# Performance work log

Hardware: AMD Instinct MI355X
Metric: run time of the kernel (lower is better)

Reference implementation:

```python
import jax, jax.numpy as jnp
import numpy as np

B, S, IN_DIM, D_MODEL, H = 8, 1024, 512, 1024, 16
DEPTH = D_MODEL // H
LN_EPS = 1e-5


def setup_inputs() -> dict:
    key = jax.random.key(0)
    ks = jax.random.split(key, 10)
    def xavier(k, shape):
        fan_in, fan_out = shape[0], shape[1]
        lim = float(np.sqrt(6.0 / (fan_in + fan_out)))
        return jax.random.uniform(k, shape, jnp.float32, -lim, lim)
    return {
        "x": jax.random.normal(ks[0], (B, S, IN_DIM), jnp.float32),
        "mask": jax.random.randint(ks[1], (H, S, S), 0, 2, jnp.int32),
        "wq_w": xavier(ks[2], (IN_DIM, D_MODEL)),
        "wq_b": jnp.zeros((D_MODEL,), jnp.float32),
        "wk_w": xavier(ks[3], (IN_DIM, D_MODEL)),
        "wk_b": jnp.zeros((D_MODEL,), jnp.float32),
        "wv_w": xavier(ks[4], (IN_DIM, D_MODEL)),
        "wv_b": jnp.zeros((D_MODEL,), jnp.float32),
        "dense_w": xavier(ks[5], (D_MODEL, D_MODEL)),
        "dense_b": jnp.zeros((D_MODEL,), jnp.float32),
        "res_w": xavier(ks[6], (IN_DIM, D_MODEL)),  # residual_linear (no bias)
        "ln_g": 1.0 + 0.02 * jax.random.normal(ks[7], (D_MODEL,), jnp.float32),
        "ln_b": 0.02 * jax.random.normal(ks[8], (D_MODEL,), jnp.float32),
    }


def reference(x, mask, wq_w, wq_b, wk_w, wk_b, wv_w, wv_b,
              dense_w, dense_b, res_w, ln_g, ln_b):
    bs = x.shape[0]
    residual = x @ res_w  # [B,S,D_MODEL]
    # project and split heads -> [B,H,S,depth]
    def split(t):
        return t.reshape(bs, -1, H, DEPTH).transpose(0, 2, 1, 3)
    q = split(x @ wq_w + wq_b)
    k = split(x @ wk_w + wk_b)
    v = split(x @ wv_w + wv_b)
    scale = 1.0 / jnp.sqrt(jnp.asarray(DEPTH, x.dtype))
    attn = jnp.einsum("bhqd,bhkd->bhqk", q, k) * scale
    attn = jnp.where(mask[None] == 0, jnp.asarray(-1e9, attn.dtype), attn)
    attn = jax.nn.softmax(attn, axis=-1)  # dropout is identity in eval
    out = jnp.einsum("bhqk,bhkd->bhqd", attn, v)
    out = out.transpose(0, 2, 1, 3).reshape(bs, -1, D_MODEL)
    out = out @ dense_w + dense_b
    # residual + LayerNorm
    y = residual + out
    mu = jnp.mean(y, axis=-1, keepdims=True)
    var = jnp.mean(jnp.square(y - mu), axis=-1, keepdims=True)
    y = (y - mu) * jax.lax.rsqrt(var + LN_EPS)
    return y * ln_g + ln_b
```

## Files before the change

### kernel.cpp

```cpp
#include <hip/hip_runtime.h>
#include <stdint.h>

#define B_ 8
#define S_ 1024
#define IN_DIM 512
#define DM 1024
#define H_ 16
#define DEP 64

typedef __bf16 bf16;
typedef __attribute__((ext_vector_type(8))) __bf16 bf16x8;
typedef __attribute__((ext_vector_type(4))) __bf16 bf16x4;
typedef __attribute__((ext_vector_type(4))) short short4v;
typedef __attribute__((ext_vector_type(4))) float f32x4;

#if defined(__has_builtin)
#if __has_builtin(__builtin_amdgcn_mfma_f32_16x16x16_bf16)
#define HAVE_NEW16 1
#endif
#endif
static __device__ __forceinline__ f32x4 mfma16(bf16x4 a, bf16x4 b, f32x4 c) {
#ifdef HAVE_NEW16
    return __builtin_amdgcn_mfma_f32_16x16x16_bf16(a, b, c, 0, 0, 0);
#else
    union { bf16x4 h; short4v s; } ua, ub;
    ua.h = a; ub.h = b;
    return __builtin_amdgcn_mfma_f32_16x16x16bf16_1k(ua.s, ub.s, c, 0, 0, 0);
#endif
}

static __device__ __forceinline__ void gld_lds16(const void* g, void* l) {
    __builtin_amdgcn_global_load_lds(
        (const __attribute__((address_space(1))) uint32_t*)g,
        (__attribute__((address_space(3))) uint32_t*)l, 16, 0, 0);
}

__global__ void detect_kernel(const uint16_t* __restrict__ xraw, int* __restrict__ flag) {
    const int t = threadIdx.x;
    int sane = 0;
    #pragma unroll
    for (int j = 0; j < 8; j++) {
        const uint16_t u = xraw[t * 8 + j];
        const int e = (u >> 7) & 0xff;
        sane += ((u & 0x7fff) == 0 || (e >= 100 && e <= 140)) ? 1 : 0;
    }
    #pragma unroll
    for (int m = 1; m < 64; m <<= 1) sane += __shfl_xor(sane, m);
    if (t == 0) *flag = (sane >= 450) ? 1 : 0;
}

static __device__ __forceinline__ float ldin(const void* p, size_t i, int isb) {
    return isb ? (float)((const bf16*)p)[i] : ((const float*)p)[i];
}

__global__ __launch_bounds__(256) void transpose_kernel(
    const void* __restrict__ wq, const void* __restrict__ wk, const void* __restrict__ wv,
    const void* __restrict__ res, const void* __restrict__ dense,
    bf16* __restrict__ wqT, bf16* __restrict__ wkT, bf16* __restrict__ wvT,
    bf16* __restrict__ resT, bf16* __restrict__ denseT, const int* __restrict__ flag)
{
    const int isb = *flag;
    __shared__ bf16 tile[32][33];
    const int z = blockIdx.z;
    const void* src; bf16* dst; int kb, kd;
    if (z == 0)      { src = wq;    dst = wqT;    kb = 0;   kd = 512;  }
    else if (z == 1) { src = wk;    dst = wkT;    kb = 0;   kd = 512;  }
    else if (z == 2) { src = wv;    dst = wvT;    kb = 0;   kd = 512;  }
    else if (z == 3) { src = res;   dst = resT;   kb = 0;   kd = 512;  }
    else if (z == 4) { src = dense; dst = denseT; kb = 0;   kd = 1024; }
    else             { src = dense; dst = denseT; kb = 512; kd = 1024; }
    const int n0 = blockIdx.x * 32, k0 = blockIdx.y * 32;
    const int tx = threadIdx.x, ty = threadIdx.y;
    #pragma unroll
    for (int r = 0; r < 4; r++)
        tile[ty + r*8][tx] = (bf16)ldin(src, (size_t)(kb + k0 + ty + r*8) * DM + n0 + tx, isb);
    __syncthreads();
    #pragma unroll
    for (int r = 0; r < 4; r++)
        dst[(size_t)(n0 + ty + r*8) * kd + kb + k0 + tx] = tile[tx][ty + r*8];
}

__global__ __launch_bounds__(256) void xconv_kernel(
    const void* __restrict__ x, bf16* __restrict__ xc, const int* __restrict__ flag)
{
    const int isb = *flag;
    const size_t i = ((size_t)blockIdx.x * 256 + threadIdx.x) * 4;
    #pragma unroll
    for (int j = 0; j < 4; j++) xc[i + j] = (bf16)ldin(x, i + j, isb);
}

__global__ __launch_bounds__(256) void smallconv_kernel(
    const void* b0, const void* b1, const void* b2, const void* b3,
    const void* b4, const void* b5, bf16* __restrict__ out, const int* __restrict__ flag)
{
    const int isb = *flag;
    const void* srcs[6] = {b0, b1, b2, b3, b4, b5};
    const void* s = srcs[blockIdx.x];
    for (int i = threadIdx.x; i < 1024; i += 256)
        out[blockIdx.x * 1024 + i] = (bf16)ldin(s, i, isb);
}

__global__ __launch_bounds__(256) void maskpack_kernel(
    const int* __restrict__ mask, unsigned long long* __restrict__ mb)
{
    const int w = threadIdx.x >> 6, lane = threadIdx.x & 63;
    const int gw = blockIdx.x * 4 + w;
    for (int c = gw; c < 262144; c += 4096) {
        const int v = mask[(size_t)c * 64 + lane];
        const unsigned long long bits = __ballot(v != 0);
        if (lane == 0) mb[c] = bits;
    }
}

template<int KDIM>
static __device__ __forceinline__ void gemm_core(
    const bf16* __restrict__ A, const bf16* __restrict__ BT,
    int m0, int n0, bf16* Asm, bf16* Bsm, f32x4 acc[4][4])
{
    const int tid = threadIdx.x, l = tid & 63, w = tid >> 6;
    const int wm = w >> 1, wn = w & 1, quad = l >> 4, l15 = l & 15;
    #pragma unroll
    for (int i = 0; i < 4; i++)
        #pragma unroll
        for (int j = 0; j < 4; j++) acc[i][j] = f32x4{0.f, 0.f, 0.f, 0.f};

    for (int k0 = 0; k0 < KDIM; k0 += 32) {
        __syncthreads();
        #pragma unroll
        for (int qq = 0; qq < 2; qq++) {
            const int c = qq*256 + tid;
            const int row = c >> 2, ch = c & 3;
            gld_lds16(A  + (size_t)(m0 + row)*KDIM + k0 + ch*8, Asm + (qq*256 + w*64)*8);
            gld_lds16(BT + (size_t)(n0 + row)*KDIM + k0 + ch*8, Bsm + (qq*256 + w*64)*8);
        }
        __syncthreads();
        bf16x8 af[4], bfv[4];
        #pragma unroll
        for (int i = 0; i < 4; i++)
            af[i] = *(const bf16x8*)(Asm + (wm*64 + i*16 + l15)*32 + quad*8);
        #pragma unroll
        for (int j = 0; j < 4; j++)
            bfv[j] = *(const bf16x8*)(Bsm + (wn*64 + j*16 + l15)*32 + quad*8);
        #pragma unroll
        for (int i = 0; i < 4; i++)
            #pragma unroll
            for (int j = 0; j < 4; j++)
                acc[i][j] = __builtin_amdgcn_mfma_f32_16x16x32_bf16(af[i], bfv[j], acc[i][j], 0, 0, 0);
    }
}

#define EPI_P 132
__global__ __launch_bounds__(256) void proj_kernel(
    const bf16* __restrict__ x,
    const bf16* __restrict__ wqT, const bf16* __restrict__ wkT,
    const bf16* __restrict__ wvT, const bf16* __restrict__ resT,
    const bf16* __restrict__ small,
    bf16* __restrict__ Q, bf16* __restrict__ K, bf16* __restrict__ VtG, bf16* __restrict__ R)
{
    __shared__ alignas(16) char smem[17408];
    bf16* Asm = (bf16*)smem;
    bf16* Bsm = (bf16*)(smem + 8192);
    bf16* epi = (bf16*)smem;

    const int m0 = blockIdx.x * 128;
    const int ng = blockIdx.y * 128;
    const int sel = ng >> 10, n0 = ng & 1023;
    const bf16* BT; const bf16* bias = nullptr;
    if (sel == 0)      { BT = wqT; bias = small;        }
    else if (sel == 1) { BT = wkT; bias = small + 1024; }
    else if (sel == 2) { BT = wvT; bias = small + 2048; }
    else               { BT = resT; }

    f32x4 acc[4][4];
    gemm_core<IN_DIM>(x, BT, m0, n0, Asm, Bsm, acc);

    const int tid = threadIdx.x, l = tid & 63, w = tid >> 6;
    const int wm = w >> 1, wn = w & 1, quad = l >> 4, l15 = l & 15;

    if (sel == 2) {
        const int bb = m0 >> 10, srow0 = m0 & 1023;
        #pragma unroll
        for (int hf = 0; hf < 2; hf++) {
            __syncthreads();
            if (wn == hf) {
                #pragma unroll
                for (int j = 0; j < 4; j++) {
                    const int cl = j*16 + l15;
                    const float bv = (float)bias[n0 + hf*64 + cl];
                    #pragma unroll
                    for (int i = 0; i < 4; i++) {
                        const int rho = wm*64 + i*16 + quad*4;
                        #pragma unroll
                        for (int r = 0; r < 4; r++)
                            epi[cl*EPI_P + rho + r] = (bf16)(acc[i][j][r] + bv);
                    }
                }
            }
            __syncthreads();
            const int hh = (n0 >> 6) + hf;
            const int sc = tid & 15;
            #pragma unroll
            for (int pass = 0; pass < 4; pass++) {
                const int dl = (tid >> 4) + pass*16;
                bf16x8 v;
                #pragma unroll
                for (int k = 0; k < 8; k++) v[k] = epi[dl*EPI_P + sc*8 + k];
                *(bf16x8*)(VtG + ((size_t)(bb*16 + hh)*64 + dl)*S_ + srow0 + sc*8) = v;
            }
        }
        return;
    }

    #pragma unroll
    for (int j = 0; j < 4; j++) {
        const int col = n0 + wn*64 + j*16 + l15;
        const float bv = (sel < 3) ? (float)bias[col] : 0.f;
        #pragma unroll
        for (int i = 0; i < 4; i++) {
            const int rb = m0 + wm*64 + i*16 + quad*4;
            #pragma unroll
            for (int r = 0; r < 4; r++) {
                const float v = acc[i][j][r] + bv;
                if (sel == 0)      Q[(size_t)(rb + r)*DM + col] = (bf16)(v * 0.125f);
                else if (sel == 1) K[(size_t)(rb + r)*DM + col] = (bf16)v;
                else               R[(size_t)(rb + r)*DM + col] = (bf16)v;
            }
        }
    }
}

#define KP 68
__global__ __launch_bounds__(256) void attn_kernel(
    const bf16* __restrict__ Q, const bf16* __restrict__ K, const bf16* __restrict__ VtG,
    const unsigned long long* __restrict__ mb, bf16* __restrict__ AO)
{
    __shared__ alignas(16) bf16 Ksm[64*KP];
    __shared__ alignas(16) bf16 Vsm[64*KP];

    const int tid = threadIdx.x, l = tid & 63, w = tid >> 6;
    const int quad = l >> 4, l15 = l & 15;
    const int b = blockIdx.y >> 4, h = blockIdx.y & 15;
    const int wrow = blockIdx.x*128 + w*32;
    const size_t rowbase = (size_t)b * S_;

    bf16x8 qa[2][2];
    #pragma unroll
    for (int g = 0; g < 2; g++) {
        const bf16* qp = Q + (rowbase + wrow + g*16 + l15)*DM + h*DEP + quad*8;
        qa[g][0] = *(const bf16x8*)qp;
        qa[g][1] = *(const bf16x8*)(qp + 32);
    }
    const bf16* kgbase = K + rowbase*DM + h*DEP;
    const bf16* vgbase = VtG + (size_t)(b*16 + h)*64*S_;
    const unsigned long long* mbase[2];
    #pragma unroll
    for (int g = 0; g < 2; g++)
        mbase[g] = mb + ((size_t)h*S_ + wrow + g*16 + l15) * 16;

    f32x4 oT[2][4];
    float lsum[2] = {0.f, 0.f};
    #pragma unroll
    for (int g = 0; g < 2; g++)
        #pragma unroll
        for (int dt = 0; dt < 4; dt++) oT[g][dt] = f32x4{0.f,0.f,0.f,0.f};

    const int srow = tid >> 3, sch = tid & 7;

    bf16x8 k0v = *(const bf16x8*)(kgbase + (size_t)srow*DM + sch*8);
    bf16x8 k1v = *(const bf16x8*)(kgbase + (size_t)(32 + srow)*DM + sch*8);
    bf16x8 v0v = *(const bf16x8*)(vgbase + (size_t)srow*S_ + sch*8);
    bf16x8 v1v = *(const bf16x8*)(vgbase + (size_t)(32 + srow)*S_ + sch*8);
    uint32_t mlo[2], mhi[2];
    #pragma unroll
    for (int g = 0; g < 2; g++) {
        const unsigned long long mword = mbase[g][0];
        mlo[g] = (uint32_t)mword; mhi[g] = (uint32_t)(mword >> 32);
    }

    for (int it = 0; it < 16; it++) {
        __syncthreads();
        *(bf16x8*)(Ksm + srow*KP + sch*8)        = k0v;
        *(bf16x8*)(Ksm + (32 + srow)*KP + sch*8) = k1v;
        *(bf16x8*)(Vsm + srow*KP + sch*8)        = v0v;
        *(bf16x8*)(Vsm + (32 + srow)*KP + sch*8) = v1v;
        __syncthreads();

        const uint32_t cmlo[2] = {mlo[0], mlo[1]}, cmhi[2] = {mhi[0], mhi[1]};
        if (it + 1 < 16) {
            const int nkt = (it + 1) * 64;
            k0v = *(const bf16x8*)(kgbase + (size_t)(nkt + srow)*DM + sch*8);
            k1v = *(const bf16x8*)(kgbase + (size_t)(nkt + 32 + srow)*DM + sch*8);
            v0v = *(const bf16x8*)(vgbase + (size_t)srow*S_ + nkt + sch*8);
            v1v = *(const bf16x8*)(vgbase + (size_t)(32 + srow)*S_ + nkt + sch*8);
            #pragma unroll
            for (int g = 0; g < 2; g++) {
                const unsigned long long mword = mbase[g][it + 1];
                mlo[g] = (uint32_t)mword; mhi[g] = (uint32_t)(mword >> 32);
            }
        }

        #pragma unroll
        for (int sub = 0; sub < 2; sub++) {
            bf16x8 kf[2][2];
            bf16x4 va[2][4];
            #pragma unroll
            for (int h2 = 0; h2 < 2; h2++) {
                const bf16* kp = Ksm + (sub*32 + h2*16 + l15)*KP + quad*8;
                kf[h2][0] = *(const bf16x8*)kp;
                kf[h2][1] = *(const bf16x8*)(kp + 32);
            }
            #pragma unroll
            for (int h2 = 0; h2 < 2; h2++)
                #pragma unroll
                for (int dt = 0; dt < 4; dt++)
                    va[h2][dt] = *(const bf16x4*)(Vsm + (dt*16 + l15)*KP + sub*32 + h2*16 + quad*4);

            #pragma unroll
            for (int g = 0; g < 2; g++) {
                f32x4 st[2];
                #pragma unroll
                for (int h2 = 0; h2 < 2; h2++) {
                    f32x4 z = {0.f,0.f,0.f,0.f};
                    z = __builtin_amdgcn_mfma_f32_16x16x32_bf16(kf[h2][0], qa[g][0], z, 0, 0, 0);
                    z = __builtin_amdgcn_mfma_f32_16x16x32_bf16(kf[h2][1], qa[g][1], z, 0, 0, 0);
                    st[h2] = z;
                }
                const uint32_t msk = sub ? cmhi[g] : cmlo[g];
                bf16x4 pb[2];
                #pragma unroll
                for (int h2 = 0; h2 < 2; h2++) {
                    const uint32_t nib = (msk >> (h2*16 + quad*4)) & 0xfu;
                    #pragma unroll
                    for (int r = 0; r < 4; r++) {
                        const float e = __expf(st[h2][r]);
                        const float pv = ((nib >> r) & 1u) ? e : 0.f;
                        lsum[g] += pv;
                        pb[h2][r] = (bf16)pv;
                    }
                }
                #pragma unroll
                for (int h2 = 0; h2 < 2; h2++)
                    #pragma unroll
                    for (int dt = 0; dt < 4; dt++)
                        oT[g][dt] = mfma16(va[h2][dt], pb[h2], oT[g][dt]);
            }
        }
    }

    #pragma unroll
    for (int g = 0; g < 2; g++) {
        lsum[g] += __shfl_xor(lsum[g], 16);
        lsum[g] += __shfl_xor(lsum[g], 32);
        const float inv = 1.0f / lsum[g];
        bf16* aor = AO + (rowbase + wrow + g*16 + l15)*DM + h*DEP;
        #pragma unroll
        for (int dt = 0; dt < 4; dt++) {
            bf16x4 ov;
            #pragma unroll
            for (int r = 0; r < 4; r++) ov[r] = (bf16)(oT[g][dt][r] * inv);
            *(bf16x4*)(aor + dt*16 + quad*4) = ov;
        }
    }
}

__global__ __launch_bounds__(256) void dense_kernel(
    const bf16* __restrict__ AOin, const bf16* __restrict__ dT,
    const bf16* __restrict__ db, bf16* __restrict__ R)
{
    __shared__ alignas(16) bf16 Asm[128*32];
    __shared__ alignas(16) bf16 Bsm[128*32];
    const int m0 = blockIdx.x * 128, n0 = blockIdx.y * 128;
    f32x4 acc[4][4];
    gemm_core<DM>(AOin, dT, m0, n0, Asm, Bsm, acc);
    const int tid = threadIdx.x, l = tid & 63, w = tid >> 6;
    const int wm = w >> 1, wn = w & 1, quad = l >> 4, l15 = l & 15;
    #pragma unroll
    for (int j = 0; j < 4; j++) {
        const int col = n0 + wn*64 + j*16 + l15;
        const float bv = (float)db[col];
        #pragma unroll
        for (int i = 0; i < 4; i++) {
            const int rb = m0 + wm*64 + i*16 + quad*4;
            #pragma unroll
            for (int r = 0; r < 4; r++) {
                const size_t idx = (size_t)(rb + r)*DM + col;
                R[idx] = (bf16)((float)R[idx] + acc[i][j][r] + bv);
            }
        }
    }
}

__global__ __launch_bounds__(256) void ln_kernel(
    const bf16* __restrict__ R, const bf16* __restrict__ small,
    void* __restrict__ out, const int* __restrict__ flag)
{
    const int isb = *flag;
    __shared__ float red[8];
    const int row = blockIdx.x, tid = threadIdx.x;
    const bf16x4 rv = *(const bf16x4*)(R + (size_t)row*DM + tid*4);
    const float vx = (float)rv[0], vy = (float)rv[1], vz = (float)rv[2], vw = (float)rv[3];
    float s = vx + vy + vz + vw;
    #pragma unroll
    for (int m = 1; m < 64; m <<= 1) s += __shfl_xor(s, m);
    const int w = tid >> 6;
    if ((tid & 63) == 0) red[w] = s;
    __syncthreads();
    const float mu = (red[0] + red[1] + red[2] + red[3]) * (1.0f/DM);
    const float dx = vx - mu, dy = vy - mu, dz = vz - mu, dw = vw - mu;
    float q = dx*dx + dy*dy + dz*dz + dw*dw;
    #pragma unroll
    for (int m = 1; m < 64; m <<= 1) q += __shfl_xor(q, m);
    if ((tid & 63) == 0) red[4 + w] = q;
    __syncthreads();
    const float var = (red[4] + red[5] + red[6] + red[7]) * (1.0f/DM);
    const float rstd = rsqrtf(var + 1e-5f);
    const int col = tid * 4;
    const bf16x4 gv = *(const bf16x4*)(small + 4*1024 + col);
    const bf16x4 bv = *(const bf16x4*)(small + 5*1024 + col);
    const float o0 = dx*rstd*(float)gv[0] + (float)bv[0];
    const float o1 = dy*rstd*(float)gv[1] + (float)bv[1];
    const float o2 = dz*rstd*(float)gv[2] + (float)bv[2];
    const float o3 = dw*rstd*(float)gv[3] + (float)bv[3];
    if (isb) {
        bf16x4 ov; ov[0] = (bf16)o0; ov[1] = (bf16)o1; ov[2] = (bf16)o2; ov[3] = (bf16)o3;
        *(bf16x4*)((bf16*)out + (size_t)row*DM + col) = ov;
    } else {
        float4 ov = {o0, o1, o2, o3};
        *(float4*)((float*)out + (size_t)row*DM + col) = ov;
    }
}

extern "C" void kernel_launch(void* const* d_in, const int* in_sizes, int n_in,
                              void* d_out, int out_size, void* d_ws, size_t ws_size,
                              hipStream_t stream) {
    const int* mask = (const int*)d_in[1];

    char* ws = (char*)d_ws;
    bf16* wqT   = (bf16*)(ws);
    bf16* wkT   = (bf16*)(ws + ((size_t)1 << 20));
    bf16* wvT   = (bf16*)(ws + ((size_t)2 << 20));
    bf16* resT  = (bf16*)(ws + ((size_t)3 << 20));
    bf16* dT    = (bf16*)(ws + ((size_t)4 << 20));
    bf16* small = (bf16*)(ws + ((size_t)6 << 20));
    int*  flag  = (int*) (ws + ((size_t)6 << 20) + 16384);
    unsigned long long* mbits = (unsigned long long*)(ws + ((size_t)7 << 20));
    bf16* Qb    = (bf16*)(ws + ((size_t)9  << 20));
    bf16* Kb    = (bf16*)(ws + ((size_t)25 << 20));
    bf16* VtG   = (bf16*)(ws + ((size_t)41 << 20));
    bf16* R     = (bf16*)(ws + ((size_t)57 << 20));
    bf16* xc    = (bf16*)d_out;

    detect_kernel<<<1, 64, 0, stream>>>((const uint16_t*)d_in[0], flag);
    transpose_kernel<<<dim3(32, 16, 6), dim3(32, 8), 0, stream>>>(
        d_in[2], d_in[4], d_in[6], d_in[10], d_in[8],
        wqT, wkT, wvT, resT, dT, flag);
    xconv_kernel<<<4096, 256, 0, stream>>>(d_in[0], xc, flag);
    smallconv_kernel<<<6, 256, 0, stream>>>(
        d_in[3], d_in[5], d_in[7], d_in[9], d_in[11], d_in[12], small, flag);
    maskpack_kernel<<<1024, 256, 0, stream>>>(mask, mbits);
    proj_kernel<<<dim3(64, 32), 256, 0, stream>>>(
        xc, wqT, wkT, wvT, resT, small, Qb, Kb, VtG, R);
    attn_kernel<<<dim3(8, 128), 256, 0, stream>>>(Qb, Kb, VtG, mbits, Qb );
    dense_kernel<<<dim3(64, 8), 256, 0, stream>>>(Qb, dT, small + 3*1024, R);
    ln_kernel<<<8192, 256, 0, stream>>>(R, small, d_out, flag);
}
```

Measured before the change: 370.3 us.

## Double-buffer attention K/V tiles, use exp2, MFMA row sums, XCD-aware block mapping

The attention kernel now double-buffers its K/V shared-memory tiles, which removes one barrier per iteration and stores the prefetched tile into the other buffer after compute. Q is pre-scaled by log2(e)/8 so the kernel can call the hardware exp2 directly, and the softmax denominator is accumulated with an extra MFMA against a ones vector instead of scalar adds and cross-lane shuffles. Blocks are remapped so that consecutive block IDs on the same XCD share a batch-head, which is meant to improve L2 reuse of K/V. It also adds an occupancy hint in the launch bounds and a simplified mask bit test. The costs are double the LDS per block, extra MFMA work, and possible register pressure from the occupancy bound.

```diff
diff --git a/kernel.cpp b/kernel.cpp
--- a/kernel.cpp
+++ b/kernel.cpp
@@ -221,7 +221,7 @@
             #pragma unroll
             for (int r = 0; r < 4; r++) {
                 const float v = acc[i][j][r] + bv;
-                if (sel == 0)      Q[(size_t)(rb + r)*DM + col] = (bf16)(v * 0.125f);
+                if (sel == 0)      Q[(size_t)(rb + r)*DM + col] = (bf16)(v * 0.18033688f);
                 else if (sel == 1) K[(size_t)(rb + r)*DM + col] = (bf16)v;
                 else               R[(size_t)(rb + r)*DM + col] = (bf16)v;
             }
@@ -230,17 +230,22 @@
 }
 
 #define KP 68
-__global__ __launch_bounds__(256) void attn_kernel(
+__global__ __launch_bounds__(256, 4) void attn_kernel(
     const bf16* __restrict__ Q, const bf16* __restrict__ K, const bf16* __restrict__ VtG,
     const unsigned long long* __restrict__ mb, bf16* __restrict__ AO)
 {
-    __shared__ alignas(16) bf16 Ksm[64*KP];
-    __shared__ alignas(16) bf16 Vsm[64*KP];
+    __shared__ alignas(16) bf16 Ksm[2*64*KP];
+    __shared__ alignas(16) bf16 Vsm[2*64*KP];
 
     const int tid = threadIdx.x, l = tid & 63, w = tid >> 6;
     const int quad = l >> 4, l15 = l & 15;
-    const int b = blockIdx.y >> 4, h = blockIdx.y & 15;
-    const int wrow = blockIdx.x*128 + w*32;
+
+    const int fid = blockIdx.y * 8 + blockIdx.x;
+    const int xcd = fid & 7, idx = fid >> 3;
+    const int bh  = xcd * 16 + (idx >> 3);
+    const int qt  = idx & 7;
+    const int b = bh >> 4, h = bh & 15;
+    const int wrow = qt*128 + w*32;
     const size_t rowbase = (size_t)b * S_;
 
     bf16x8 qa[2][2];
@@ -257,19 +262,33 @@
     for (int g = 0; g < 2; g++)
         mbase[g] = mb + ((size_t)h*S_ + wrow + g*16 + l15) * 16;
 
+    uint32_t bmr[4];
+    #pragma unroll
+    for (int r = 0; r < 4; r++) bmr[r] = 1u << (quad*4 + r);
+
+    bf16x4 onesv;
+    #pragma unroll
+    for (int r = 0; r < 4; r++) onesv[r] = (bf16)1.0f;
+
     f32x4 oT[2][4];
-    float lsum[2] = {0.f, 0.f};
-    #pragma unroll
-    for (int g = 0; g < 2; g++)
+    f32x4 lacc[2];
+    #pragma unroll
+    for (int g = 0; g < 2; g++) {
+        lacc[g] = f32x4{0.f,0.f,0.f,0.f};
         #pragma unroll
         for (int dt = 0; dt < 4; dt++) oT[g][dt] = f32x4{0.f,0.f,0.f,0.f};
+    }
 
     const int srow = tid >> 3, sch = tid & 7;
-
-    bf16x8 k0v = *(const bf16x8*)(kgbase + (size_t)srow*DM + sch*8);
-    bf16x8 k1v = *(const bf16x8*)(kgbase + (size_t)(32 + srow)*DM + sch*8);
-    bf16x8 v0v = *(const bf16x8*)(vgbase + (size_t)srow*S_ + sch*8);
-    bf16x8 v1v = *(const bf16x8*)(vgbase + (size_t)(32 + srow)*S_ + sch*8);
+    const bf16* kg0 = kgbase + (size_t)srow*DM + sch*8;
+    const bf16* kg1 = kgbase + (size_t)(32 + srow)*DM + sch*8;
+    const bf16* vg0 = vgbase + (size_t)srow*S_ + sch*8;
+    const bf16* vg1 = vgbase + (size_t)(32 + srow)*S_ + sch*8;
+
+    bf16x8 k0v = *(const bf16x8*)kg0;
+    bf16x8 k1v = *(const bf16x8*)kg1;
+    bf16x8 v0v = *(const bf16x8*)vg0;
+    bf16x8 v1v = *(const bf16x8*)vg1;
     uint32_t mlo[2], mhi[2];
     #pragma unroll
     for (int g = 0; g < 2; g++) {
@@ -277,21 +296,26 @@
         mlo[g] = (uint32_t)mword; mhi[g] = (uint32_t)(mword >> 32);
     }
 
+    *(bf16x8*)(Ksm + srow*KP + sch*8)        = k0v;
+    *(bf16x8*)(Ksm + (32 + srow)*KP + sch*8) = k1v;
+    *(bf16x8*)(Vsm + srow*KP + sch*8)        = v0v;
+    *(bf16x8*)(Vsm + (32 + srow)*KP + sch*8) = v1v;
+
     for (int it = 0; it < 16; it++) {
-        __syncthreads();
-        *(bf16x8*)(Ksm + srow*KP + sch*8)        = k0v;
-        *(bf16x8*)(Ksm + (32 + srow)*KP + sch*8) = k1v;
-        *(bf16x8*)(Vsm + srow*KP + sch*8)        = v0v;
-        *(bf16x8*)(Vsm + (32 + srow)*KP + sch*8) = v1v;
+        const int cur = (it & 1) * (64*KP);
+        const int nxt = ((it & 1) ^ 1) * (64*KP);
+        const bf16* Kc = Ksm + cur;
+        const bf16* Vc = Vsm + cur;
         __syncthreads();
 
         const uint32_t cmlo[2] = {mlo[0], mlo[1]}, cmhi[2] = {mhi[0], mhi[1]};
         if (it + 1 < 16) {
-            const int nkt = (it + 1) * 64;
-            k0v = *(const bf16x8*)(kgbase + (size_t)(nkt + srow)*DM + sch*8);
-            k1v = *(const bf16x8*)(kgbase + (size_t)(nkt + 32 + srow)*DM + sch*8);
-            v0v = *(const bf16x8*)(vgbase + (size_t)srow*S_ + nkt + sch*8);
-            v1v = *(const bf16x8*)(vgbase + (size_t)(32 + srow)*S_ + nkt + sch*8);
+            const size_t ko = (size_t)(it + 1) * 64 * DM;
+            const int    vo = (it + 1) * 64;
+            k0v = *(const bf16x8*)(kg0 + ko);
+            k1v = *(const bf16x8*)(kg1 + ko);
+            v0v = *(const bf16x8*)(vg0 + vo);
+            v1v = *(const bf16x8*)(vg1 + vo);
             #pragma unroll
             for (int g = 0; g < 2; g++) {
                 const unsigned long long mword = mbase[g][it + 1];
@@ -305,7 +329,7 @@
             bf16x4 va[2][4];
             #pragma unroll
             for (int h2 = 0; h2 < 2; h2++) {
-                const bf16* kp = Ksm + (sub*32 + h2*16 + l15)*KP + quad*8;
+                const bf16* kp = Kc + (sub*32 + h2*16 + l15)*KP + quad*8;
                 kf[h2][0] = *(const bf16x8*)kp;
                 kf[h2][1] = *(const bf16x8*)(kp + 32);
             }
@@ -313,7 +337,7 @@
             for (int h2 = 0; h2 < 2; h2++)
                 #pragma unroll
                 for (int dt = 0; dt < 4; dt++)
-                    va[h2][dt] = *(const bf16x4*)(Vsm + (dt*16 + l15)*KP + sub*32 + h2*16 + quad*4);
+                    va[h2][dt] = *(const bf16x4*)(Vc + (dt*16 + l15)*KP + sub*32 + h2*16 + quad*4);
 
             #pragma unroll
             for (int g = 0; g < 2; g++) {
@@ -329,29 +353,35 @@
                 bf16x4 pb[2];
                 #pragma unroll
                 for (int h2 = 0; h2 < 2; h2++) {
-                    const uint32_t nib = (msk >> (h2*16 + quad*4)) & 0xfu;
+                    const uint32_t mh = msk >> (h2 * 16);
                     #pragma unroll
                     for (int r = 0; r < 4; r++) {
-                        const float e = __expf(st[h2][r]);
-                        const float pv = ((nib >> r) & 1u) ? e : 0.f;
-                        lsum[g] += pv;
+                        const float e = __builtin_amdgcn_exp2f(st[h2][r]);
+                        const float pv = (mh & bmr[r]) ? e : 0.f;
                         pb[h2][r] = (bf16)pv;
                     }
                 }
                 #pragma unroll
-                for (int h2 = 0; h2 < 2; h2++)
+                for (int h2 = 0; h2 < 2; h2++) {
+                    lacc[g] = mfma16(onesv, pb[h2], lacc[g]);
                     #pragma unroll
                     for (int dt = 0; dt < 4; dt++)
                         oT[g][dt] = mfma16(va[h2][dt], pb[h2], oT[g][dt]);
-            }
+                }
+            }
+        }
+
+        if (it + 1 < 16) {
+            *(bf16x8*)(Ksm + nxt + srow*KP + sch*8)        = k0v;
+            *(bf16x8*)(Ksm + nxt + (32 + srow)*KP + sch*8) = k1v;
+            *(bf16x8*)(Vsm + nxt + srow*KP + sch*8)        = v0v;
+            *(bf16x8*)(Vsm + nxt + (32 + srow)*KP + sch*8) = v1v;
         }
     }
 
     #pragma unroll
     for (int g = 0; g < 2; g++) {
-        lsum[g] += __shfl_xor(lsum[g], 16);
-        lsum[g] += __shfl_xor(lsum[g], 32);
-        const float inv = 1.0f / lsum[g];
+        const float inv = 1.0f / lacc[g][0];
         bf16* aor = AO + (rowbase + wrow + g*16 + l15)*DM + h*DEP;
         #pragma unroll
         for (int dt = 0; dt < 4; dt++) {
```

After: 364.6 us. About the same (-1.6%).
